# Optimization experiments

Hardware: AMD Instinct MI355X
Metric: run time of the kernel (lower is better)

Reference implementation:

```python
import jax, jax.numpy as jnp
import numpy as np

N = 8192
F_IN = 256
F_OUT = 64
ALPHA = 0.2  # LeakyReLU negative slope
NEG_INF = -9e15


def setup_inputs() -> dict:
    key = jax.random.key(0)
    k1, k2, k3, k4 = jax.random.split(key, 4)
    h = jax.random.normal(k1, (N, F_IN), dtype=jnp.float32)
    adj = jax.random.randint(k2, (N, N), 0, 2, dtype=jnp.int32)
    W = jax.random.normal(k3, (F_IN, F_OUT), dtype=jnp.float32) * 0.1
    a = jax.random.normal(k4, (2 * F_OUT, 1), dtype=jnp.float32) * 0.1
    return {"h": h, "adj": adj, "W": W, "a": a}


def reference(h, adj, W, a):
    # Wh: [N, F_out]
    Wh = h @ W
    # e_ij = LeakyReLU(a1 . Wh_i + a2 . Wh_j); same math as the O(N^2*2F)
    # concat in the original, computed via two [N] gathers + broadcast add.
    f_src = Wh @ a[:F_OUT, 0]   # [N] contribution of node i (row)
    f_dst = Wh @ a[F_OUT:, 0]   # [N] contribution of node j (col)
    e = f_src[:, None] + f_dst[None, :]          # [N, N]
    e = jnp.where(e > 0, e, ALPHA * e)           # LeakyReLU
    # masked softmax over neighbors (dim=1)
    e = jnp.where(adj > 0, e, NEG_INF)
    attention = jax.nn.softmax(e, axis=1)        # [N, N]
    h_prime = attention @ Wh                     # [N, F_out]
    # concat=True -> ELU
    return jax.nn.elu(h_prime)
```

## Files before the change

kernel.cpp:

```cpp
#include <hip/hip_runtime.h>
#include <math.h>

#define N 8192
#define FIN 256
#define FOUT 64
#define ALPHA 0.2f
#define LOG2E 1.442695040888963f

#define MPITCH 260
#define SMEM_BYTES 33280

typedef float f32x4 __attribute__((ext_vector_type(4)));
typedef _Float16 f16x8 __attribute__((ext_vector_type(8)));

union F16V { uint4 u; f16x8 h; };

__device__ __forceinline__ unsigned pack_f16(float a, float b) {
    union { _Float16 h; unsigned short u; } ca, cb;
    ca.h = (_Float16)a; cb.h = (_Float16)b;
    return (unsigned)ca.u | ((unsigned)cb.u << 16);
}
__device__ __forceinline__ float wcalc(unsigned av, float fsr, float g) {
    float e = fsr + g;
    float le = e > 0.f ? e : ALPHA * e;
    float r = __builtin_exp2f(fmaf(le, LOG2E, -4.0f));
    return av != 0u ? r : 0.f;
}

__global__ __launch_bounds__(512) void gat_prep(
    const float* __restrict__ h, const float* __restrict__ W,
    const float* __restrict__ a, const int* __restrict__ adj,
    float* __restrict__ fsrc, float* __restrict__ fdst,
    uint4* __restrict__ Bp, unsigned char* __restrict__ mask8)
{
    __shared__ float sWh[32][FOUT + 1];
    const int t = threadIdx.x;

    if (blockIdx.x >= 256) {
        const size_t tid = (size_t)(blockIdx.x - 256) * 512 + t;
        const int4 v0 = *reinterpret_cast<const int4*>(&adj[tid * 8]);
        const int4 v1 = *reinterpret_cast<const int4*>(&adj[tid * 8 + 4]);
        unsigned m = 0;
        m |= (v0.x != 0) ? 1u : 0u;
        m |= (v0.y != 0) ? 2u : 0u;
        m |= (v0.z != 0) ? 4u : 0u;
        m |= (v0.w != 0) ? 8u : 0u;
        m |= (v1.x != 0) ? 16u : 0u;
        m |= (v1.y != 0) ? 32u : 0u;
        m |= (v1.z != 0) ? 64u : 0u;
        m |= (v1.w != 0) ? 128u : 0u;
        mask8[tid] = (unsigned char)m;
        return;
    }

    const int f = t & 63;
    const int wq = t >> 6;
    const int row0 = blockIdx.x * 32;
    const int rbase = row0 + wq * 4;

    float acc[4] = {0.f, 0.f, 0.f, 0.f};
    for (int k0 = 0; k0 < FIN; k0 += 4) {
        const float w0 = W[(k0 + 0) * FOUT + f];
        const float w1 = W[(k0 + 1) * FOUT + f];
        const float w2 = W[(k0 + 2) * FOUT + f];
        const float w3 = W[(k0 + 3) * FOUT + f];
#pragma unroll
        for (int rr = 0; rr < 4; ++rr) {
            const float4 hv = *reinterpret_cast<const float4*>(
                &h[(size_t)(rbase + rr) * FIN + k0]);
            acc[rr] = fmaf(hv.x, w0, acc[rr]);
            acc[rr] = fmaf(hv.y, w1, acc[rr]);
            acc[rr] = fmaf(hv.z, w2, acc[rr]);
            acc[rr] = fmaf(hv.w, w3, acc[rr]);
        }
    }
    const float as = a[f], ad = a[FOUT + f];
#pragma unroll
    for (int rr = 0; rr < 4; ++rr) {
        sWh[wq * 4 + rr][f] = acc[rr];
        float fs = acc[rr] * as, fd = acc[rr] * ad;
#pragma unroll
        for (int off = 1; off < 64; off <<= 1) {
            fs += __shfl_xor(fs, off, 64);
            fd += __shfl_xor(fd, off, 64);
        }
        if (f == 0) { fsrc[rbase + rr] = fs; fdst[rbase + rr] = fd; }
    }
    __syncthreads();
    if (t < 256) {
        const int ft = t >> 6;
        const int l = t & 63;
        const int li = l & 15, g = l >> 4;
        float v[8];
#pragma unroll
        for (int e = 0; e < 8; ++e) v[e] = sWh[g * 8 + e][ft * 16 + li];
        uint4 pk;
        pk.x = pack_f16(v[0], v[1]);
        pk.y = pack_f16(v[2], v[3]);
        pk.z = pack_f16(v[4], v[5]);
        pk.w = pack_f16(v[6], v[7]);
        Bp[(size_t)(blockIdx.x * 4 + ft) * 64 + l] = pk;
    }
}

struct Regs { unsigned mw; float4 g0, g1; uint4 b0, b1, b2, b3; };

__global__ __launch_bounds__(512, 4) void gat_main(
    const unsigned char* __restrict__ mask8,
    const uint4* __restrict__ Bp,
    const float* __restrict__ fsrc, const float* __restrict__ fdst,
    float* __restrict__ out)
{
    __shared__ __align__(16) char smem[SMEM_BYTES];
    unsigned* M32 = reinterpret_cast<unsigned*>(smem);

    const int t = threadIdx.x;
    const int l = t & 63;
    const int w = t >> 6;
    const int row0 = blockIdx.x * 16;

    const int r = l & 15;
    const int g16 = l >> 4;
    const int kg8 = g16 << 3;
    const int jwbase = w * 1024;
    const int cgbase = w * 32;
    const float fsr = fsrc[row0 + r];
    const int mbase = r * MPITCH + w * 32;
    const int shft = g16 * 8;

    const uint4 s0 = *reinterpret_cast<const uint4*>(&mask8[(size_t)row0 * 1024 + t * 32]);
    const uint4 s1 = *reinterpret_cast<const uint4*>(&mask8[(size_t)row0 * 1024 + t * 32 + 16]);

    f32x4 acc0 = {0.f, 0.f, 0.f, 0.f};
    f32x4 acc1 = {0.f, 0.f, 0.f, 0.f};
    f32x4 acc2 = {0.f, 0.f, 0.f, 0.f};
    f32x4 acc3 = {0.f, 0.f, 0.f, 0.f};
    float zacc = 0.f;
    Regs RA, RB;

#define LOADG(c, S)                                                            \
    {                                                                          \
        const int j0_ = jwbase + (c) * 32;                                     \
        S.g0 = *reinterpret_cast<const float4*>(&fdst[j0_ + kg8]);             \
        S.g1 = *reinterpret_cast<const float4*>(&fdst[j0_ + kg8 + 4]);         \
        const uint4* bp_ = Bp + (size_t)(cgbase + (c)) * 4 * 64 + l;           \
        S.b0 = bp_[0];                                                         \
        S.b1 = bp_[64];                                                        \
        S.b2 = bp_[128];                                                       \
        S.b3 = bp_[192];                                                       \
    }

#define MREAD(c, S) { S.mw = M32[mbase + (c)]; }

#define COMPUTE(S)                                                             \
    {                                                                          \
        const unsigned m8 = (S.mw >> shft) & 0xffu;                            \
        const float w0 = wcalc(m8 & 1u,   fsr, S.g0.x);                        \
        const float w1 = wcalc(m8 & 2u,   fsr, S.g0.y);                        \
        const float w2 = wcalc(m8 & 4u,   fsr, S.g0.z);                        \
        const float w3 = wcalc(m8 & 8u,   fsr, S.g0.w);                        \
        const float w4 = wcalc(m8 & 16u,  fsr, S.g1.x);                        \
        const float w5 = wcalc(m8 & 32u,  fsr, S.g1.y);                        \
        const float w6 = wcalc(m8 & 64u,  fsr, S.g1.z);                        \
        const float w7 = wcalc(m8 & 128u, fsr, S.g1.w);                        \
        zacc += (w0 + w1) + (w2 + w3) + ((w4 + w5) + (w6 + w7));               \
        F16V av, b0v, b1v, b2v, b3v;                                           \
        av.u.x = pack_f16(w0, w1); av.u.y = pack_f16(w2, w3);                  \
        av.u.z = pack_f16(w4, w5); av.u.w = pack_f16(w6, w7);                  \
        b0v.u = S.b0; b1v.u = S.b1; b2v.u = S.b2; b3v.u = S.b3;                \
        __builtin_amdgcn_s_setprio(1);                                         \
        acc0 = __builtin_amdgcn_mfma_f32_16x16x32_f16(av.h, b0v.h, acc0, 0, 0, 0); \
        acc1 = __builtin_amdgcn_mfma_f32_16x16x32_f16(av.h, b1v.h, acc1, 0, 0, 0); \
        acc2 = __builtin_amdgcn_mfma_f32_16x16x32_f16(av.h, b2v.h, acc2, 0, 0, 0); \
        acc3 = __builtin_amdgcn_mfma_f32_16x16x32_f16(av.h, b3v.h, acc3, 0, 0, 0); \
        __builtin_amdgcn_s_setprio(0);                                         \
    }

    LOADG(0, RA);
    LOADG(1, RB);

    {
        const int mrow = t >> 5;
        const int w0i = (t & 31) * 8;
        char* dst = smem + (mrow * MPITCH + w0i) * 4;
        *reinterpret_cast<uint4*>(dst) = s0;
        *reinterpret_cast<uint4*>(dst + 16) = s1;
    }
    asm volatile("s_waitcnt lgkmcnt(0)" ::: "memory");
    __builtin_amdgcn_s_barrier();

    MREAD(0, RA);
    MREAD(1, RB);
#pragma unroll
    for (int c = 0; c < 32; c += 2) {
        COMPUTE(RA);
        if (c + 2 < 32) { LOADG(c + 2, RA); MREAD(c + 2, RA); }
        COMPUTE(RB);
        if (c + 3 < 32) { LOADG(c + 3, RB); MREAD(c + 3, RB); }
    }
#undef LOADG
#undef MREAD
#undef COMPUTE

    float* accbuf = reinterpret_cast<float*>(smem);
    float* zbuf = reinterpret_cast<float*>(smem + 32768);
    __shared__ float Zfin[16];

    zacc += __shfl_xor(zacc, 16, 64);
    zacc += __shfl_xor(zacc, 32, 64);
    __syncthreads();
    if (l < 16) zbuf[w * 16 + l] = zacc;
    *reinterpret_cast<f32x4*>(&accbuf[((w * 4 + 0) * 64 + l) * 4]) = acc0;
    *reinterpret_cast<f32x4*>(&accbuf[((w * 4 + 1) * 64 + l) * 4]) = acc1;
    *reinterpret_cast<f32x4*>(&accbuf[((w * 4 + 2) * 64 + l) * 4]) = acc2;
    *reinterpret_cast<f32x4*>(&accbuf[((w * 4 + 3) * 64 + l) * 4]) = acc3;
    __syncthreads();
    if (t < 16) {
        float z = 0.f;
#pragma unroll
        for (int w2 = 0; w2 < 8; ++w2) z += zbuf[w2 * 16 + t];
        Zfin[t] = z;
    }
    __syncthreads();

#pragma unroll
    for (int e0 = 0; e0 < 2; ++e0) {
        const int e = t + e0 * 512;
        const int rr = e >> 6, f2 = e & 63;
        const int c = f2 >> 4;
        const int ln = (f2 & 15) | ((rr >> 2) << 4);
        const int rg = rr & 3;
        float s = 0.f;
#pragma unroll
        for (int w2 = 0; w2 < 8; ++w2)
            s += accbuf[((w2 * 4 + c) * 64 + ln) * 4 + rg];
        const float hp = s / Zfin[rr];
        out[(size_t)(row0 + rr) * FOUT + f2] = hp > 0.f ? hp : expm1f(hp);
    }
}

extern "C" void kernel_launch(void* const* d_in, const int* in_sizes, int n_in,
                              void* d_out, int out_size, void* d_ws, size_t ws_size,
                              hipStream_t stream) {
    const float* h   = (const float*)d_in[0];
    const int*   adj = (const int*)d_in[1];
    const float* W   = (const float*)d_in[2];
    const float* a   = (const float*)d_in[3];
    float* out = (float*)d_out;

    float* ws = (float*)d_ws;
    float* fsrc = ws;
    float* fdst = fsrc + N;
    uint4* Bp = (uint4*)(fdst + N);
    unsigned char* mask8 = (unsigned char*)(Bp + 65536);

    gat_prep<<<dim3(256 + 16384), dim3(512), 0, stream>>>(
        h, W, a, adj, fsrc, fdst, Bp, mask8);
    gat_main<<<dim3(N / 16), dim3(512), 0, stream>>>(
        mask8, Bp, fsrc, fdst, out);
}
```

Before: 98.52 us.

## Factor exp of LeakyReLU into per-row and per-column precomputed exponentials

Rewrites exp(leakyrelu(fs_i+fd_j)-4) as either exp(fs_i-2)*exp(fd_j-2) or exp(a*fs_i-2)*exp(a*fd_j-2). The prep kernel precomputes these per-row and per-column factors plus a threshold that selects the branch. This removes the per-element exp2 from the main loop and leaves a compare and a multiply. In exchange, each column now loads twice as much data, and the main loop's full unroll pragma is dropped in favour of a peeled tail, which may change the schedule.

```diff
diff --git a/kernel.cpp b/kernel.cpp
--- a/kernel.cpp
+++ b/kernel.cpp
@@ -5,7 +5,6 @@
 #define FIN 256
 #define FOUT 64
 #define ALPHA 0.2f
-#define LOG2E 1.442695040888963f
 
 #define MPITCH 260
 #define SMEM_BYTES 33280
@@ -20,17 +19,12 @@
     ca.h = (_Float16)a; cb.h = (_Float16)b;
     return (unsigned)ca.u | ((unsigned)cb.u << 16);
 }
-__device__ __forceinline__ float wcalc(unsigned av, float fsr, float g) {
-    float e = fsr + g;
-    float le = e > 0.f ? e : ALPHA * e;
-    float r = __builtin_exp2f(fmaf(le, LOG2E, -4.0f));
-    return av != 0u ? r : 0.f;
-}
 
 __global__ __launch_bounds__(512) void gat_prep(
     const float* __restrict__ h, const float* __restrict__ W,
     const float* __restrict__ a, const int* __restrict__ adj,
-    float* __restrict__ fsrc, float* __restrict__ fdst,
+    float* __restrict__ Arow, float* __restrict__ Crow, float* __restrict__ Thr,
+    float2* __restrict__ BD,
     uint4* __restrict__ Bp, unsigned char* __restrict__ mask8)
 {
     __shared__ float sWh[32][FOUT + 1];
@@ -84,7 +78,13 @@
             fs += __shfl_xor(fs, off, 64);
             fd += __shfl_xor(fd, off, 64);
         }
-        if (f == 0) { fsrc[rbase + rr] = fs; fdst[rbase + rr] = fd; }
+        if (f == 0) {
+            const int row = rbase + rr;
+            Arow[row] = expf(fs - 2.0f);
+            Crow[row] = expf(ALPHA * fs - 2.0f);
+            Thr[row]  = expf(-fs - 2.0f);
+            BD[row] = make_float2(expf(fd - 2.0f), expf(ALPHA * fd - 2.0f));
+        }
     }
     __syncthreads();
     if (t < 256) {
@@ -103,12 +103,13 @@
     }
 }
 
-struct Regs { unsigned mw; float4 g0, g1; uint4 b0, b1, b2, b3; };
+struct Regs { unsigned mw; float4 bd0, bd1, bd2, bd3; uint4 b0, b1, b2, b3; };
 
 __global__ __launch_bounds__(512, 4) void gat_main(
     const unsigned char* __restrict__ mask8,
     const uint4* __restrict__ Bp,
-    const float* __restrict__ fsrc, const float* __restrict__ fdst,
+    const float* __restrict__ Arow, const float* __restrict__ Crow,
+    const float* __restrict__ Thr, const float2* __restrict__ BD,
     float* __restrict__ out)
 {
     __shared__ __align__(16) char smem[SMEM_BYTES];
@@ -124,9 +125,12 @@
     const int kg8 = g16 << 3;
     const int jwbase = w * 1024;
     const int cgbase = w * 32;
-    const float fsr = fsrc[row0 + r];
+    const float Ai = Arow[row0 + r];
+    const float Ci = Crow[row0 + r];
+    const float thr = Thr[row0 + r];
     const int mbase = r * MPITCH + w * 32;
     const int shft = g16 * 8;
+    const float* BDf = reinterpret_cast<const float*>(BD);
 
     const uint4 s0 = *reinterpret_cast<const uint4*>(&mask8[(size_t)row0 * 1024 + t * 32]);
     const uint4 s1 = *reinterpret_cast<const uint4*>(&mask8[(size_t)row0 * 1024 + t * 32 + 16]);
@@ -140,9 +144,11 @@
 
 #define LOADG(c, S)                                                            \
     {                                                                          \
-        const int j0_ = jwbase + (c) * 32;                                     \
-        S.g0 = *reinterpret_cast<const float4*>(&fdst[j0_ + kg8]);             \
-        S.g1 = *reinterpret_cast<const float4*>(&fdst[j0_ + kg8 + 4]);         \
+        const int jf_ = (jwbase + (c) * 32 + kg8) * 2;  \
+        S.bd0 = *reinterpret_cast<const float4*>(&BDf[jf_]);                   \
+        S.bd1 = *reinterpret_cast<const float4*>(&BDf[jf_ + 4]);               \
+        S.bd2 = *reinterpret_cast<const float4*>(&BDf[jf_ + 8]);               \
+        S.bd3 = *reinterpret_cast<const float4*>(&BDf[jf_ + 12]);              \
         const uint4* bp_ = Bp + (size_t)(cgbase + (c)) * 4 * 64 + l;           \
         S.b0 = bp_[0];                                                         \
         S.b1 = bp_[64];                                                        \
@@ -152,17 +158,20 @@
 
 #define MREAD(c, S) { S.mw = M32[mbase + (c)]; }
 
+#define WC(B_, D_, bit_) \
+    ((((m8 & (bit_)) != 0u)) ? (((B_) > thr) ? Ai * (B_) : Ci * (D_)) : 0.f)
+
 #define COMPUTE(S)                                                             \
     {                                                                          \
         const unsigned m8 = (S.mw >> shft) & 0xffu;                            \
-        const float w0 = wcalc(m8 & 1u,   fsr, S.g0.x);                        \
-        const float w1 = wcalc(m8 & 2u,   fsr, S.g0.y);                        \
-        const float w2 = wcalc(m8 & 4u,   fsr, S.g0.z);                        \
-        const float w3 = wcalc(m8 & 8u,   fsr, S.g0.w);                        \
-        const float w4 = wcalc(m8 & 16u,  fsr, S.g1.x);                        \
-        const float w5 = wcalc(m8 & 32u,  fsr, S.g1.y);                        \
-        const float w6 = wcalc(m8 & 64u,  fsr, S.g1.z);                        \
-        const float w7 = wcalc(m8 & 128u, fsr, S.g1.w);                        \
+        const float w0 = WC(S.bd0.x, S.bd0.y, 1u);                             \
+        const float w1 = WC(S.bd0.z, S.bd0.w, 2u);                             \
+        const float w2 = WC(S.bd1.x, S.bd1.y, 4u);                             \
+        const float w3 = WC(S.bd1.z, S.bd1.w, 8u);                             \
+        const float w4 = WC(S.bd2.x, S.bd2.y, 16u);                            \
+        const float w5 = WC(S.bd2.z, S.bd2.w, 32u);                            \
+        const float w6 = WC(S.bd3.x, S.bd3.y, 64u);                            \
+        const float w7 = WC(S.bd3.z, S.bd3.w, 128u);                           \
         zacc += (w0 + w1) + (w2 + w3) + ((w4 + w5) + (w6 + w7));               \
         F16V av, b0v, b1v, b2v, b3v;                                           \
         av.u.x = pack_f16(w0, w1); av.u.y = pack_f16(w2, w3);                  \
@@ -191,15 +200,17 @@
 
     MREAD(0, RA);
     MREAD(1, RB);
-#pragma unroll
-    for (int c = 0; c < 32; c += 2) {
+    for (int c = 0; c < 30; c += 2) {
         COMPUTE(RA);
-        if (c + 2 < 32) { LOADG(c + 2, RA); MREAD(c + 2, RA); }
+        LOADG(c + 2, RA); MREAD(c + 2, RA);
         COMPUTE(RB);
-        if (c + 3 < 32) { LOADG(c + 3, RB); MREAD(c + 3, RB); }
-    }
+        LOADG(c + 3, RB); MREAD(c + 3, RB);
+    }
+    COMPUTE(RA);
+    COMPUTE(RB);
 #undef LOADG
 #undef MREAD
+#undef WC
 #undef COMPUTE
 
     float* accbuf = reinterpret_cast<float*>(smem);
@@ -249,13 +260,15 @@
     float* out = (float*)d_out;
 
     float* ws = (float*)d_ws;
-    float* fsrc = ws;
-    float* fdst = fsrc + N;
-    uint4* Bp = (uint4*)(fdst + N);
+    float* Arow = ws;
+    float* Crow = Arow + N;
+    float* Thr  = Crow + N;
+    float2* BD  = (float2*)(Thr + N);
+    uint4* Bp = (uint4*)(BD + N);
     unsigned char* mask8 = (unsigned char*)(Bp + 65536);
 
     gat_prep<<<dim3(256 + 16384), dim3(512), 0, stream>>>(
-        h, W, a, adj, fsrc, fdst, Bp, mask8);
+        h, W, a, adj, Arow, Crow, Thr, BD, Bp, mask8);
     gat_main<<<dim3(N / 16), dim3(512), 0, stream>>>(
-        mask8, Bp, fsrc, fdst, out);
-}
+        mask8, Bp, Arow, Crow, Thr, BD, out);
+}
```

New measurement: 99.10 us. No clear change (+0.6%).
